# Optimization experiments

Measured on AMD Instinct MI355X. Metric: run time of the kernel, lower is better.

Reference implementation:

```python
import jax, jax.numpy as jnp
import numpy as np

CHUNK_SIZE = 1024  # module default chunk_size


def setup_inputs() -> dict:
    key = jax.random.key(0)
    kq, kk, kv = jax.random.split(key, 3)
    B, H, S, D = 2, 16, 2048, 64
    q = jax.random.normal(kq, (B, H, S, D), dtype=jnp.float32)
    k = jax.random.normal(kk, (B, H, S, D), dtype=jnp.float32)
    v = jax.random.normal(kv, (B, H, S, D), dtype=jnp.float32)
    return {"q": q, "k": k, "v": v}


def reference(q, k, v):
    # Chunked causal attention: q split into chunks of CHUNK_SIZE along seq,
    # each chunk attends to the full K/V with causal mask (tril, diagonal=start).
    B, H, S, D = q.shape
    scale = D ** (-0.5)
    cs = CHUNK_SIZE
    nc = S // cs  # S is a multiple of chunk_size here
    qc = q.reshape(B, H, nc, cs, D)
    # scores: [B, H, nc, cs, S]
    scores = jnp.einsum('bhncd,bhsd->bhncs', qc, k) * scale
    # causal mask per chunk: key position j visible iff j <= chunk_start + i
    row = (jnp.arange(nc) * cs)[:, None, None] + jnp.arange(cs)[None, :, None]  # [nc, cs, 1]
    col = jnp.arange(S)[None, None, :]  # [1, 1, S]
    causal = col <= row  # [nc, cs, S]
    scores = jnp.where(causal[None, None], scores, -jnp.inf)
    attn = jax.nn.softmax(scores, axis=-1)
    out = jnp.einsum('bhncs,bhsd->bhncd', attn, v)
    return out.reshape(B, H, S, D)
```

## Files before the change

kernel.cpp:

```cpp
#include <hip/hip_runtime.h>

typedef __bf16 bf16x8 __attribute__((ext_vector_type(8)));
typedef float f32x4 __attribute__((ext_vector_type(4)));

#define S_LEN 2048
#define D_DIM 64

__global__ __launch_bounds__(256, 4) void attn_fwd(const float* __restrict__ Q,
                                                   const float* __restrict__ K,
                                                   const float* __restrict__ V,
                                                   float* __restrict__ O) {
    const int b    = blockIdx.x;
    const int xcd  = b & 7;
    const int cs   = (b >> 3) & 31;
    const int j    = b >> 8;
    const int head = xcd * 4 + (cs >> 3);
    const int slot = cs & 7;
    const int chunk = (j == 0) ? slot : (j == 1) ? (31 - slot)
                    : (j == 2) ? (slot + 8) : (23 - slot);

    const int tid  = threadIdx.x;
    const int wave = tid >> 6;
    const int lane = tid & 63;
    const int l15  = lane & 15;
    const int lhi  = lane >> 4;

    const int q0 = chunk * 64 + wave * 16;
    const size_t base = (size_t)head * (S_LEN * D_DIM);
    const float qscale = 0.125f * 1.44269504088896340736f;

    __shared__ __align__(16) __bf16 Klds[2][64][64];
    __shared__ __align__(16) __bf16 Vt[2][64][64];
    __shared__ __align__(16) __bf16 Plds[4][16][64];

    const int rk = tid >> 2;
    const int ck = (tid & 3) << 4;
    const int kp = tid & 31;
    const int dc = tid >> 5;
    const int swk = (rk & 7) << 3;

    bf16x8 qf[2];
    {
        const float* qrow = Q + base + (size_t)(q0 + l15) * D_DIM + lhi * 8;
        #pragma unroll
        for (int h = 0; h < 2; ++h) {
            f32x4 a = *(const f32x4*)(qrow + h * 32);
            f32x4 bq = *(const f32x4*)(qrow + h * 32 + 4);
            bf16x8 t;
            #pragma unroll
            for (int e = 0; e < 4; ++e) { t[e] = (__bf16)(a[e] * qscale); t[e + 4] = (__bf16)(bq[e] * qscale); }
            qf[h] = t;
        }
    }

    f32x4 acc[4];
    #pragma unroll
    for (int td = 0; td < 4; ++td) acc[td] = (f32x4){0.f, 0.f, 0.f, 0.f};
    float m_r = -1e30f, l_r = 0.f;

    f32x4 pk[4], pva[2], pvb[2];

    {
        const float* ks = K + base + (size_t)rk * D_DIM + ck;
        #pragma unroll
        for (int i = 0; i < 4; ++i) pk[i] = *(const f32x4*)(ks + 4 * i);
        const float* v0 = V + base + (size_t)(2 * kp) * D_DIM + dc * 8;
        pva[0] = *(const f32x4*)v0;           pva[1] = *(const f32x4*)(v0 + 4);
        pvb[0] = *(const f32x4*)(v0 + D_DIM); pvb[1] = *(const f32x4*)(v0 + D_DIM + 4);
        bf16x8 k0, k1;
        #pragma unroll
        for (int e = 0; e < 4; ++e) {
            k0[e] = (__bf16)pk[0][e]; k0[e + 4] = (__bf16)pk[1][e];
            k1[e] = (__bf16)pk[2][e]; k1[e + 4] = (__bf16)pk[3][e];
        }
        *(bf16x8*)&Klds[0][rk][ck ^ swk] = k0;
        *(bf16x8*)&Klds[0][rk][(ck + 8) ^ swk] = k1;
        #pragma unroll
        for (int jj = 0; jj < 8; ++jj) {
            const int d = dc * 8 + jj;
            const float av = (jj < 4) ? pva[0][jj & 3] : pva[1][jj & 3];
            const float bv = (jj < 4) ? pvb[0][jj & 3] : pvb[1][jj & 3];
            union { __bf16 h[2]; unsigned int u; } t;
            t.h[0] = (__bf16)av; t.h[1] = (__bf16)bv;
            *(unsigned int*)&Vt[0][d][(2 * kp) ^ ((d & 7) << 3)] = t.u;
        }
    }

    const int nt = chunk + 1;
    for (int kt = 0; kt < nt; ++kt) {
        const int cur = kt & 1;
        __syncthreads();

        const bool pre = (kt + 1 < nt);
        if (pre) {
            const int kv1 = (kt + 1) << 6;
            const float* ks = K + base + (size_t)(kv1 + rk) * D_DIM + ck;
            #pragma unroll
            for (int i = 0; i < 4; ++i) pk[i] = *(const f32x4*)(ks + 4 * i);
            const float* v0 = V + base + (size_t)(kv1 + 2 * kp) * D_DIM + dc * 8;
            pva[0] = *(const f32x4*)v0;           pva[1] = *(const f32x4*)(v0 + 4);
            pvb[0] = *(const f32x4*)(v0 + D_DIM); pvb[1] = *(const f32x4*)(v0 + D_DIM + 4);
        }

        f32x4 s[4];
        #pragma unroll
        for (int ct = 0; ct < 4; ++ct) s[ct] = (f32x4){0.f, 0.f, 0.f, 0.f};
        __builtin_amdgcn_s_setprio(1);
        #pragma unroll
        for (int h = 0; h < 2; ++h) {
            #pragma unroll
            for (int ct = 0; ct < 4; ++ct) {
                const int krow = ct * 16 + l15;
                bf16x8 kf = *(const bf16x8*)&Klds[cur][krow][(h * 32 + lhi * 8) ^ ((l15 & 7) << 3)];
                s[ct] = __builtin_amdgcn_mfma_f32_16x16x32_bf16(kf, qf[h], s[ct], 0, 0, 0);
            }
        }
        __builtin_amdgcn_s_setprio(0);

        if (kt == nt - 1) {
            const int kv0 = kt << 6;
            const int qg = q0 + l15;
            #pragma unroll
            for (int ct = 0; ct < 4; ++ct)
                #pragma unroll
                for (int r = 0; r < 4; ++r) {
                    const int kg = kv0 + ct * 16 + lhi * 4 + r;
                    if (kg > qg) s[ct][r] = -1e30f;
                }
        }

        float mm = fmaxf(fmaxf(fmaxf(s[0][0], s[0][1]), fmaxf(s[0][2], s[0][3])),
                         fmaxf(fmaxf(s[1][0], s[1][1]), fmaxf(s[1][2], s[1][3])));
        mm = fmaxf(mm, fmaxf(fmaxf(fmaxf(s[2][0], s[2][1]), fmaxf(s[2][2], s[2][3])),
                             fmaxf(fmaxf(s[3][0], s[3][1]), fmaxf(s[3][2], s[3][3]))));
        mm = fmaxf(mm, __shfl_xor(mm, 16));
        mm = fmaxf(mm, __shfl_xor(mm, 32));
        if (!__all(mm - m_r <= 8.0f)) {
            const float mn = fmaxf(m_r, mm);
            const float f = exp2f(m_r - mn);
            m_r = mn;
            l_r *= f;
            #pragma unroll
            for (int r = 0; r < 4; ++r) {
                const float fr = __shfl(f, lhi * 4 + r);
                #pragma unroll
                for (int td = 0; td < 4; ++td) acc[td][r] *= fr;
            }
        }
        float ps = 0.f;
        #pragma unroll
        for (int ct = 0; ct < 4; ++ct)
            #pragma unroll
            for (int r = 0; r < 4; ++r) {
                const float p = exp2f(s[ct][r] - m_r);
                s[ct][r] = p;
                ps += p;
            }
        ps += __shfl_xor(ps, 16);
        ps += __shfl_xor(ps, 32);
        l_r += ps;

        #pragma unroll
        for (int ct = 0; ct < 4; ++ct) {
            union { __bf16 h[4]; unsigned long long u; } pw;
            #pragma unroll
            for (int r = 0; r < 4; ++r) pw.h[r] = (__bf16)s[ct][r];
            *(unsigned long long*)&Plds[wave][l15][(ct * 16 + lhi * 4) ^ ((l15 & 7) << 3)] = pw.u;
        }
        asm volatile("s_waitcnt lgkmcnt(0)" ::: "memory");
        bf16x8 pf[2];
        #pragma unroll
        for (int kh = 0; kh < 2; ++kh)
            pf[kh] = *(const bf16x8*)&Plds[wave][l15][(kh * 32 + lhi * 8) ^ ((l15 & 7) << 3)];
        asm volatile("" ::: "memory");

        __builtin_amdgcn_s_setprio(1);
        #pragma unroll
        for (int kh = 0; kh < 2; ++kh) {
            #pragma unroll
            for (int td = 0; td < 4; ++td) {
                const int vrow = td * 16 + l15;
                bf16x8 vf = *(const bf16x8*)&Vt[cur][vrow][(kh * 32 + lhi * 8) ^ ((vrow & 7) << 3)];
                acc[td] = __builtin_amdgcn_mfma_f32_16x16x32_bf16(pf[kh], vf, acc[td], 0, 0, 0);
            }
        }
        __builtin_amdgcn_s_setprio(0);

        if (pre) {
            const int nxt = cur ^ 1;
            bf16x8 k0, k1;
            #pragma unroll
            for (int e = 0; e < 4; ++e) {
                k0[e] = (__bf16)pk[0][e]; k0[e + 4] = (__bf16)pk[1][e];
                k1[e] = (__bf16)pk[2][e]; k1[e + 4] = (__bf16)pk[3][e];
            }
            *(bf16x8*)&Klds[nxt][rk][ck ^ swk] = k0;
            *(bf16x8*)&Klds[nxt][rk][(ck + 8) ^ swk] = k1;
            #pragma unroll
            for (int jj = 0; jj < 8; ++jj) {
                const int d = dc * 8 + jj;
                const float av = (jj < 4) ? pva[0][jj & 3] : pva[1][jj & 3];
                const float bv = (jj < 4) ? pvb[0][jj & 3] : pvb[1][jj & 3];
                union { __bf16 h[2]; unsigned int u; } t;
                t.h[0] = (__bf16)av; t.h[1] = (__bf16)bv;
                *(unsigned int*)&Vt[nxt][d][(2 * kp) ^ ((d & 7) << 3)] = t.u;
            }
        }
    }

    float* orow = O + base + (size_t)q0 * D_DIM;
    #pragma unroll
    for (int r = 0; r < 4; ++r) {
        const float inv = 1.0f / __shfl(l_r, lhi * 4 + r);
        #pragma unroll
        for (int td = 0; td < 4; ++td)
            orow[(size_t)(lhi * 4 + r) * D_DIM + td * 16 + l15] = acc[td][r] * inv;
    }
}

extern "C" void kernel_launch(void* const* d_in, const int* in_sizes, int n_in,
                              void* d_out, int out_size, void* d_ws, size_t ws_size,
                              hipStream_t stream) {
    const float* q = (const float*)d_in[0];
    const float* k = (const float*)d_in[1];
    const float* v = (const float*)d_in[2];
    float* o = (float*)d_out;
    attn_fwd<<<dim3(1024), dim3(256), 0, stream>>>(q, k, v, o);
}
```

Before: 58.46 us.

## Pre-convert K/V to bf16 in workspace and stream tiles via global_load_lds

Adds a pre-pass kernel that converts K to bf16 and V to a transposed bf16 layout in the workspace. The attention kernel then fills its LDS double buffers with direct global-to-LDS loads, dropping the per-tile fp32 loads, register conversion and scattered transpose stores. This is meant to halve the K/V bytes the main kernel reads and remove VALU and LDS-store work from its loop. In exchange it costs an extra launch and a full write/read of the converted copies. The old kernel is kept as a fallback when the workspace is too small.

```diff
diff --git a/kernel.cpp b/kernel.cpp
--- a/kernel.cpp
+++ b/kernel.cpp
@@ -5,10 +5,61 @@
 
 #define S_LEN 2048
 #define D_DIM 64
+#define NHEAD 32
+
+typedef __attribute__((address_space(1))) const void gas;
+typedef __attribute__((address_space(3))) void las;
+
+__global__ __launch_bounds__(256) void convert_kv(const float* __restrict__ K,
+                                                  const float* __restrict__ V,
+                                                  __bf16* __restrict__ Kb,
+                                                  __bf16* __restrict__ Vtg) {
+    const int head = blockIdx.y;
+    const int s0   = blockIdx.x * 64;
+    const int tr   = threadIdx.x >> 2;
+    const int tc   = (threadIdx.x & 3) << 4;
+    const size_t ib = (size_t)head * (S_LEN * D_DIM) + (size_t)(s0 + tr) * D_DIM + tc;
+
+    __shared__ __bf16 tb[64][72];
+
+    {
+        const float* kr = K + ib;
+        f32x4 a = *(const f32x4*)kr, b = *(const f32x4*)(kr + 4),
+              c = *(const f32x4*)(kr + 8), d = *(const f32x4*)(kr + 12);
+        bf16x8 o0, o1;
+        #pragma unroll
+        for (int e = 0; e < 4; ++e) {
+            o0[e] = (__bf16)a[e]; o0[e + 4] = (__bf16)b[e];
+            o1[e] = (__bf16)c[e]; o1[e + 4] = (__bf16)d[e];
+        }
+        __bf16* ko = Kb + ib;
+        *(bf16x8*)ko = o0; *(bf16x8*)(ko + 8) = o1;
+    }
+    {
+        const float* vr = V + ib;
+        f32x4 a = *(const f32x4*)vr, b = *(const f32x4*)(vr + 4),
+              c = *(const f32x4*)(vr + 8), d = *(const f32x4*)(vr + 12);
+        #pragma unroll
+        for (int e = 0; e < 4; ++e) {
+            tb[tc +  e][tr] = (__bf16)a[e];
+            tb[tc + 4 + e][tr] = (__bf16)b[e];
+            tb[tc + 8 + e][tr] = (__bf16)c[e];
+            tb[tc + 12 + e][tr] = (__bf16)d[e];
+        }
+    }
+    __syncthreads();
+    {
+        bf16x8 o0, o1;
+        #pragma unroll
+        for (int e = 0; e < 8; ++e) { o0[e] = tb[tr][tc + e]; o1[e] = tb[tr][tc + 8 + e]; }
+        __bf16* vo = Vtg + (size_t)head * (D_DIM * S_LEN) + (size_t)tr * S_LEN + s0 + tc;
+        *(bf16x8*)vo = o0; *(bf16x8*)(vo + 8) = o1;
+    }
+}
 
 __global__ __launch_bounds__(256, 4) void attn_fwd(const float* __restrict__ Q,
-                                                   const float* __restrict__ K,
-                                                   const float* __restrict__ V,
+                                                   const __bf16* __restrict__ Kb,
+                                                   const __bf16* __restrict__ Vg,
                                                    float* __restrict__ O) {
     const int b    = blockIdx.x;
     const int xcd  = b & 7;
@@ -26,22 +77,23 @@
     const int lhi  = lane >> 4;
 
     const int q0 = chunk * 64 + wave * 16;
-    const size_t base = (size_t)head * (S_LEN * D_DIM);
+    const size_t qbase = (size_t)head * (S_LEN * D_DIM);
+    const size_t vbase = (size_t)head * (D_DIM * S_LEN);
     const float qscale = 0.125f * 1.44269504088896340736f;
 
     __shared__ __align__(16) __bf16 Klds[2][64][64];
     __shared__ __align__(16) __bf16 Vt[2][64][64];
     __shared__ __align__(16) __bf16 Plds[4][16][64];
 
-    const int rk = tid >> 2;
-    const int ck = (tid & 3) << 4;
-    const int kp = tid & 31;
-    const int dc = tid >> 5;
-    const int swk = (rk & 7) << 3;
+    const int xsw = (lane & 7) ^ ((lane >> 3) & 7);
+    const size_t kOff = (size_t)(lane >> 3) * D_DIM + (size_t)xsw * 8;
+    const size_t vOff = (size_t)(lane >> 3) * S_LEN + (size_t)xsw * 8;
+    const __bf16* kgw = Kb + qbase + (size_t)(wave * 16) * D_DIM + kOff;
+    const __bf16* vgw = Vg + vbase + (size_t)(wave * 16) * S_LEN + vOff;
 
     bf16x8 qf[2];
     {
-        const float* qrow = Q + base + (size_t)(q0 + l15) * D_DIM + lhi * 8;
+        const float* qrow = Q + qbase + (size_t)(q0 + l15) * D_DIM + lhi * 8;
         #pragma unroll
         for (int h = 0; h < 2; ++h) {
             f32x4 a = *(const f32x4*)(qrow + h * 32);
@@ -58,49 +110,24 @@
     for (int td = 0; td < 4; ++td) acc[td] = (f32x4){0.f, 0.f, 0.f, 0.f};
     float m_r = -1e30f, l_r = 0.f;
 
-    f32x4 pk[4], pva[2], pvb[2];
-
-    {
-        const float* ks = K + base + (size_t)rk * D_DIM + ck;
-        #pragma unroll
-        for (int i = 0; i < 4; ++i) pk[i] = *(const f32x4*)(ks + 4 * i);
-        const float* v0 = V + base + (size_t)(2 * kp) * D_DIM + dc * 8;
-        pva[0] = *(const f32x4*)v0;           pva[1] = *(const f32x4*)(v0 + 4);
-        pvb[0] = *(const f32x4*)(v0 + D_DIM); pvb[1] = *(const f32x4*)(v0 + D_DIM + 4);
-        bf16x8 k0, k1;
-        #pragma unroll
-        for (int e = 0; e < 4; ++e) {
-            k0[e] = (__bf16)pk[0][e]; k0[e + 4] = (__bf16)pk[1][e];
-            k1[e] = (__bf16)pk[2][e]; k1[e + 4] = (__bf16)pk[3][e];
-        }
-        *(bf16x8*)&Klds[0][rk][ck ^ swk] = k0;
-        *(bf16x8*)&Klds[0][rk][(ck + 8) ^ swk] = k1;
-        #pragma unroll
-        for (int jj = 0; jj < 8; ++jj) {
-            const int d = dc * 8 + jj;
-            const float av = (jj < 4) ? pva[0][jj & 3] : pva[1][jj & 3];
-            const float bv = (jj < 4) ? pvb[0][jj & 3] : pvb[1][jj & 3];
-            union { __bf16 h[2]; unsigned int u; } t;
-            t.h[0] = (__bf16)av; t.h[1] = (__bf16)bv;
-            *(unsigned int*)&Vt[0][d][(2 * kp) ^ ((d & 7) << 3)] = t.u;
-        }
-    }
+    auto stage = [&](int kv0, int bufi) {
+        const __bf16* kg = kgw + (size_t)kv0 * D_DIM;
+        const __bf16* vg = vgw + kv0;
+        __builtin_amdgcn_global_load_lds((gas*)kg,                 (las*)&Klds[bufi][wave * 16][0],     16, 0, 0);
+        __builtin_amdgcn_global_load_lds((gas*)(kg + 8 * D_DIM),   (las*)&Klds[bufi][wave * 16 + 8][0], 16, 0, 0);
+        __builtin_amdgcn_global_load_lds((gas*)vg,                 (las*)&Vt[bufi][wave * 16][0],       16, 0, 0);
+        __builtin_amdgcn_global_load_lds((gas*)(vg + 8 * S_LEN),   (las*)&Vt[bufi][wave * 16 + 8][0],   16, 0, 0);
+    };
+
+    stage(0, 0);
 
     const int nt = chunk + 1;
     for (int kt = 0; kt < nt; ++kt) {
         const int cur = kt & 1;
+        asm volatile("s_waitcnt vmcnt(0)" ::: "memory");
         __syncthreads();
 
-        const bool pre = (kt + 1 < nt);
-        if (pre) {
-            const int kv1 = (kt + 1) << 6;
-            const float* ks = K + base + (size_t)(kv1 + rk) * D_DIM + ck;
-            #pragma unroll
-            for (int i = 0; i < 4; ++i) pk[i] = *(const f32x4*)(ks + 4 * i);
-            const float* v0 = V + base + (size_t)(kv1 + 2 * kp) * D_DIM + dc * 8;
-            pva[0] = *(const f32x4*)v0;           pva[1] = *(const f32x4*)(v0 + 4);
-            pvb[0] = *(const f32x4*)(v0 + D_DIM); pvb[1] = *(const f32x4*)(v0 + D_DIM + 4);
-        }
+        if (kt + 1 < nt) stage((kt + 1) << 6, cur ^ 1);
 
         f32x4 s[4];
         #pragma unroll
@@ -185,6 +212,191 @@
             }
         }
         __builtin_amdgcn_s_setprio(0);
+    }
+
+    float* orow = O + qbase + (size_t)q0 * D_DIM;
+    #pragma unroll
+    for (int r = 0; r < 4; ++r) {
+        const float inv = 1.0f / __shfl(l_r, lhi * 4 + r);
+        #pragma unroll
+        for (int td = 0; td < 4; ++td)
+            orow[(size_t)(lhi * 4 + r) * D_DIM + td * 16 + l15] = acc[td][r] * inv;
+    }
+}
+
+__global__ __launch_bounds__(256, 4) void attn_fwd_fb(const float* __restrict__ Q,
+                                                      const float* __restrict__ K,
+                                                      const float* __restrict__ V,
+                                                      float* __restrict__ O) {
+    const int b    = blockIdx.x;
+    const int xcd  = b & 7;
+    const int cs   = (b >> 3) & 31;
+    const int j    = b >> 8;
+    const int head = xcd * 4 + (cs >> 3);
+    const int slot = cs & 7;
+    const int chunk = (j == 0) ? slot : (j == 1) ? (31 - slot)
+                    : (j == 2) ? (slot + 8) : (23 - slot);
+
+    const int tid  = threadIdx.x;
+    const int wave = tid >> 6;
+    const int lane = tid & 63;
+    const int l15  = lane & 15;
+    const int lhi  = lane >> 4;
+
+    const int q0 = chunk * 64 + wave * 16;
+    const size_t base = (size_t)head * (S_LEN * D_DIM);
+    const float qscale = 0.125f * 1.44269504088896340736f;
+
+    __shared__ __align__(16) __bf16 Klds[2][64][64];
+    __shared__ __align__(16) __bf16 Vt[2][64][64];
+    __shared__ __align__(16) __bf16 Plds[4][16][64];
+
+    const int rk = tid >> 2;
+    const int ck = (tid & 3) << 4;
+    const int kp = tid & 31;
+    const int dc = tid >> 5;
+    const int swk = (rk & 7) << 3;
+
+    bf16x8 qf[2];
+    {
+        const float* qrow = Q + base + (size_t)(q0 + l15) * D_DIM + lhi * 8;
+        #pragma unroll
+        for (int h = 0; h < 2; ++h) {
+            f32x4 a = *(const f32x4*)(qrow + h * 32);
+            f32x4 bq = *(const f32x4*)(qrow + h * 32 + 4);
+            bf16x8 t;
+            #pragma unroll
+            for (int e = 0; e < 4; ++e) { t[e] = (__bf16)(a[e] * qscale); t[e + 4] = (__bf16)(bq[e] * qscale); }
+            qf[h] = t;
+        }
+    }
+
+    f32x4 acc[4];
+    #pragma unroll
+    for (int td = 0; td < 4; ++td) acc[td] = (f32x4){0.f, 0.f, 0.f, 0.f};
+    float m_r = -1e30f, l_r = 0.f;
+
+    f32x4 pk[4], pva[2], pvb[2];
+    {
+        const float* ks = K + base + (size_t)rk * D_DIM + ck;
+        #pragma unroll
+        for (int i = 0; i < 4; ++i) pk[i] = *(const f32x4*)(ks + 4 * i);
+        const float* v0 = V + base + (size_t)(2 * kp) * D_DIM + dc * 8;
+        pva[0] = *(const f32x4*)v0;           pva[1] = *(const f32x4*)(v0 + 4);
+        pvb[0] = *(const f32x4*)(v0 + D_DIM); pvb[1] = *(const f32x4*)(v0 + D_DIM + 4);
+        bf16x8 k0, k1;
+        #pragma unroll
+        for (int e = 0; e < 4; ++e) {
+            k0[e] = (__bf16)pk[0][e]; k0[e + 4] = (__bf16)pk[1][e];
+            k1[e] = (__bf16)pk[2][e]; k1[e + 4] = (__bf16)pk[3][e];
+        }
+        *(bf16x8*)&Klds[0][rk][ck ^ swk] = k0;
+        *(bf16x8*)&Klds[0][rk][(ck + 8) ^ swk] = k1;
+        #pragma unroll
+        for (int jj = 0; jj < 8; ++jj) {
+            const int d = dc * 8 + jj;
+            const float av = (jj < 4) ? pva[0][jj & 3] : pva[1][jj & 3];
+            const float bv = (jj < 4) ? pvb[0][jj & 3] : pvb[1][jj & 3];
+            union { __bf16 h[2]; unsigned int u; } t;
+            t.h[0] = (__bf16)av; t.h[1] = (__bf16)bv;
+            *(unsigned int*)&Vt[0][d][(2 * kp) ^ ((d & 7) << 3)] = t.u;
+        }
+    }
+
+    const int nt = chunk + 1;
+    for (int kt = 0; kt < nt; ++kt) {
+        const int cur = kt & 1;
+        __syncthreads();
+        const bool pre = (kt + 1 < nt);
+        if (pre) {
+            const int kv1 = (kt + 1) << 6;
+            const float* ks = K + base + (size_t)(kv1 + rk) * D_DIM + ck;
+            #pragma unroll
+            for (int i = 0; i < 4; ++i) pk[i] = *(const f32x4*)(ks + 4 * i);
+            const float* v0 = V + base + (size_t)(kv1 + 2 * kp) * D_DIM + dc * 8;
+            pva[0] = *(const f32x4*)v0;           pva[1] = *(const f32x4*)(v0 + 4);
+            pvb[0] = *(const f32x4*)(v0 + D_DIM); pvb[1] = *(const f32x4*)(v0 + D_DIM + 4);
+        }
+
+        f32x4 s[4];
+        #pragma unroll
+        for (int ct = 0; ct < 4; ++ct) s[ct] = (f32x4){0.f, 0.f, 0.f, 0.f};
+        #pragma unroll
+        for (int h = 0; h < 2; ++h) {
+            #pragma unroll
+            for (int ct = 0; ct < 4; ++ct) {
+                const int krow = ct * 16 + l15;
+                bf16x8 kf = *(const bf16x8*)&Klds[cur][krow][(h * 32 + lhi * 8) ^ ((l15 & 7) << 3)];
+                s[ct] = __builtin_amdgcn_mfma_f32_16x16x32_bf16(kf, qf[h], s[ct], 0, 0, 0);
+            }
+        }
+
+        if (kt == nt - 1) {
+            const int kv0 = kt << 6;
+            const int qg = q0 + l15;
+            #pragma unroll
+            for (int ct = 0; ct < 4; ++ct)
+                #pragma unroll
+                for (int r = 0; r < 4; ++r) {
+                    const int kg = kv0 + ct * 16 + lhi * 4 + r;
+                    if (kg > qg) s[ct][r] = -1e30f;
+                }
+        }
+
+        float mm = fmaxf(fmaxf(fmaxf(s[0][0], s[0][1]), fmaxf(s[0][2], s[0][3])),
+                         fmaxf(fmaxf(s[1][0], s[1][1]), fmaxf(s[1][2], s[1][3])));
+        mm = fmaxf(mm, fmaxf(fmaxf(fmaxf(s[2][0], s[2][1]), fmaxf(s[2][2], s[2][3])),
+                             fmaxf(fmaxf(s[3][0], s[3][1]), fmaxf(s[3][2], s[3][3]))));
+        mm = fmaxf(mm, __shfl_xor(mm, 16));
+        mm = fmaxf(mm, __shfl_xor(mm, 32));
+        if (!__all(mm - m_r <= 8.0f)) {
+            const float mn = fmaxf(m_r, mm);
+            const float f = exp2f(m_r - mn);
+            m_r = mn;
+            l_r *= f;
+            #pragma unroll
+            for (int r = 0; r < 4; ++r) {
+                const float fr = __shfl(f, lhi * 4 + r);
+                #pragma unroll
+                for (int td = 0; td < 4; ++td) acc[td][r] *= fr;
+            }
+        }
+        float ps = 0.f;
+        #pragma unroll
+        for (int ct = 0; ct < 4; ++ct)
+            #pragma unroll
+            for (int r = 0; r < 4; ++r) {
+                const float p = exp2f(s[ct][r] - m_r);
+                s[ct][r] = p;
+                ps += p;
+            }
+        ps += __shfl_xor(ps, 16);
+        ps += __shfl_xor(ps, 32);
+        l_r += ps;
+
+        #pragma unroll
+        for (int ct = 0; ct < 4; ++ct) {
+            union { __bf16 h[4]; unsigned long long u; } pw;
+            #pragma unroll
+            for (int r = 0; r < 4; ++r) pw.h[r] = (__bf16)s[ct][r];
+            *(unsigned long long*)&Plds[wave][l15][(ct * 16 + lhi * 4) ^ ((l15 & 7) << 3)] = pw.u;
+        }
+        asm volatile("s_waitcnt lgkmcnt(0)" ::: "memory");
+        bf16x8 pf[2];
+        #pragma unroll
+        for (int kh = 0; kh < 2; ++kh)
+            pf[kh] = *(const bf16x8*)&Plds[wave][l15][(kh * 32 + lhi * 8) ^ ((l15 & 7) << 3)];
+        asm volatile("" ::: "memory");
+
+        #pragma unroll
+        for (int kh = 0; kh < 2; ++kh) {
+            #pragma unroll
+            for (int td = 0; td < 4; ++td) {
+                const int vrow = td * 16 + l15;
+                bf16x8 vf = *(const bf16x8*)&Vt[cur][vrow][(kh * 32 + lhi * 8) ^ ((vrow & 7) << 3)];
+                acc[td] = __builtin_amdgcn_mfma_f32_16x16x32_bf16(pf[kh], vf, acc[td], 0, 0, 0);
+            }
+        }
 
         if (pre) {
             const int nxt = cur ^ 1;
@@ -225,5 +437,13 @@
     const float* k = (const float*)d_in[1];
     const float* v = (const float*)d_in[2];
     float* o = (float*)d_out;
-    attn_fwd<<<dim3(1024), dim3(256), 0, stream>>>(q, k, v, o);
+    const size_t elems = (size_t)NHEAD * S_LEN * D_DIM;
+    if (ws_size >= 2 * elems * sizeof(__bf16)) {
+        __bf16* Kb  = (__bf16*)d_ws;
+        __bf16* Vtg = Kb + elems;
+        convert_kv<<<dim3(32, 32), dim3(256), 0, stream>>>(k, v, Kb, Vtg);
+        attn_fwd<<<dim3(1024), dim3(256), 0, stream>>>(q, Kb, Vtg, o);
+    } else {
+        attn_fwd_fb<<<dim3(1024), dim3(256), 0, stream>>>(q, k, v, o);
+    }
 }
```

Result: slower. 62.21 us (+6.4%).
